# Performance work log

Measured on AMD Instinct MI355X. Metric: run time of the kernel, lower is better.

The kernel has to match this reference:

```python
import math
import jax, jax.numpy as jnp
import numpy as np

EMBED_DIM = 1024
ZDIM = 128
CHUNK = 2048
DSTATE = 16
DT_RANK = math.ceil(EMBED_DIM / 16)  # 64


def silu(x):
    return x * jax.nn.sigmoid(x)


def rmsnorm(x, w, eps=1e-5):
    var = jnp.mean(x * x, axis=-1, keepdims=True)
    return x * jax.lax.rsqrt(var + eps) * w


def _rotary(v, sin, cos):
    # v: (n, d) -> rotate half
    x1, x2 = jnp.split(v, 2, axis=-1)
    return jnp.concatenate([x1 * cos - x2 * sin, x2 * cos + x1 * sin], axis=-1)


def rel_pos_bias(alpha, beta, n):
    half = ZDIM // 2
    freqs = jnp.exp(jnp.arange(half, dtype=jnp.float32) * (-math.log(10000.0) / half))
    ang = jnp.arange(n, dtype=jnp.float32)[:, None] * freqs[None, :]
    sin, cos = jnp.sin(ang), jnp.cos(ang)
    a = _rotary(jnp.broadcast_to(alpha, (n, ZDIM)), sin, cos)
    b = _rotary(jnp.broadcast_to(beta, (n, ZDIM)), sin, cos)
    return jnp.einsum('mk,nk->mn', a, b)


def s6(u, xproj_w, dt_w, dt_b, A_log, D_p):
    # Mamba-style selective scan. u: (B, L, D)
    x_dbl = u @ xproj_w.T  # (B,L,dt_rank+2*N)
    dt, Bm, Cm = jnp.split(x_dbl, [DT_RANK, DT_RANK + DSTATE], axis=-1)
    dt = jax.nn.softplus(dt @ dt_w.T + dt_b)  # (B,L,D)
    A = -jnp.exp(A_log)  # (D,N)

    def step(h, inp):
        dt_t, B_t, C_t, u_t = inp  # (B,D),(B,N),(B,N),(B,D)
        dA = jnp.exp(dt_t[..., None] * A)  # (B,D,N)
        h = dA * h + (dt_t * u_t)[..., None] * B_t[:, None, :]
        y = jnp.einsum('bdn,bn->bd', h, C_t)
        return h, y

    B, L, D = u.shape
    h0 = jnp.zeros((B, D, DSTATE), u.dtype)
    xs = (dt.transpose(1, 0, 2), Bm.transpose(1, 0, 2), Cm.transpose(1, 0, 2), u.transpose(1, 0, 2))
    _, ys = jax.lax.scan(step, h0, xs)  # ys: (L,B,D)
    return ys.transpose(1, 0, 2) + u * D_p


def setup_inputs() -> dict:
    key = jax.random.key(0)
    ks = jax.random.split(key, 12)
    std = 0.02
    B, L, D = 2, 4096, EMBED_DIM
    f32 = jnp.float32
    inp = {
        'x': jax.random.normal(ks[0], (B, L, D), f32),
        'norm_w': jnp.ones((D,), f32),
        'v_w': jax.random.normal(ks[1], (D, D), f32) * std,
        'v_b': jnp.zeros((D,), f32),
        'mx_w': jax.random.normal(ks[2], (ZDIM + D + 2 * D, D), f32) * std,
        'mx_b': jnp.zeros((ZDIM + 3 * D,), f32),
        'h_w': jax.random.normal(ks[3], (D, D), f32) * std,
        'h_b': jnp.zeros((D,), f32),
        'gamma': jax.random.normal(ks[4], (2, ZDIM), f32) * std,
        'beta': jnp.zeros((2, ZDIM), f32),
        'alpha_rb': jax.random.normal(ks[5], (1, ZDIM), f32) * std,
        'beta_rb': jax.random.normal(ks[6], (1, ZDIM), f32) * std,
        'xproj_w': jax.random.normal(ks[7], (DT_RANK + 2 * DSTATE, D), f32) * std,
        'dt_w': jax.random.normal(ks[8], (D, DT_RANK), f32) * std,
        'dt_b': jnp.full((D,), -4.6, f32),  # softplus -> dt ~ 0.01
        'A_log': jnp.log(jnp.broadcast_to(jnp.arange(1, DSTATE + 1, dtype=f32), (D, DSTATE))),
        'D_p': jnp.ones((D,), f32),
    }
    return inp


def reference(x, norm_w, v_w, v_b, mx_w, mx_b, h_w, h_b, gamma, beta,
              alpha_rb, beta_rb, xproj_w, dt_w, dt_b, A_log, D_p):
    B, L, D = x.shape
    residual = x
    xn = rmsnorm(x, norm_w)
    v = silu(xn @ v_w.T + v_b)                       # (B,L,hdim)
    mx = silu(s6(xn, xproj_w, dt_w, dt_b, A_log, D_p))
    base = mx @ mx_w.T + mx_b                        # (B,L,zdim+hdim+2D)
    u, zr, hx = jnp.split(base, [D, D + ZDIM + D], axis=-1)
    u = jax.nn.sigmoid(u)
    zr = silu(zr)
    z, r = jnp.split(zr, [ZDIM], axis=-1)
    z = z[..., None, :] * gamma + beta               # (B,L,2,Z)
    q, k = z[..., 0, :], z[..., 1, :]
    c = min(CHUNK, L)
    nc = L // c
    qh = q.reshape(B, nc, c, ZDIM) * (ZDIM ** -0.5)
    kh = k.reshape(B, nc, c, ZDIM)
    vh = v.reshape(B, nc, c, D)
    bias = rel_pos_bias(alpha_rb, beta_rb, c)        # (c,c)
    mask = jnp.triu(jnp.full((c, c), -jnp.inf, jnp.float32), 1)
    qk = jnp.einsum('bnqz,bnkz->bnqk', qh, kh) + bias + mask
    attn = jax.nn.softmax(qk.astype(jnp.float32), axis=-1).astype(qk.dtype)
    h = jnp.einsum('bnqk,bnkd->bnqd', attn, vh).reshape(B, L, D)
    h = silu(hx + (h * r) @ h_w.T + h_b)
    return residual + u * (h - residual)
```

## Files before the change

kernel.cpp:

```cpp
#include <hip/hip_runtime.h>
#include <hip/hip_bf16.h>
#include <math.h>

#define EMBED 1024
#define LSEQ 4096
#define BATCH 2
#define ZD 128
#define CHUNKC 2048
#define NSTATE 16
#define DTR 64
#define XDBL_W 96
#define NSEG 64
#define TSEG 64

typedef __attribute__((ext_vector_type(8))) short bf16x8;
typedef __attribute__((ext_vector_type(4))) float f32x4;

__device__ __forceinline__ float sigmoidf_(float x){ return 1.f/(1.f+__expf(-x)); }
__device__ __forceinline__ float siluf_(float x){ return x/(1.f+__expf(-x)); }
__device__ __forceinline__ __hip_bfloat16 tobf(float x){ return __float2bfloat16(x); }
__device__ __forceinline__ float frombf(__hip_bfloat16 x){ return __bfloat162float(x); }

__device__ __forceinline__ void gload_lds16(const void* g, void* l) {
  __builtin_amdgcn_global_load_lds(
      (const __attribute__((address_space(1))) unsigned int*)g,
      (__attribute__((address_space(3))) unsigned int*)l, 16, 0, 0);
}

__global__ __launch_bounds__(256) void prep_k(
    const float* __restrict__ v_w, const float* __restrict__ xproj_w,
    const float* __restrict__ h_w, const float* __restrict__ dt_w,
    const float* __restrict__ mx_w,
    const float* __restrict__ alpha, const float* __restrict__ beta,
    __hip_bfloat16* __restrict__ wcat, __hip_bfloat16* __restrict__ hwb,
    __hip_bfloat16* __restrict__ dtwb, __hip_bfloat16* __restrict__ mxwb,
    float* __restrict__ gtab)
{
  int b = blockIdx.x, tid = threadIdx.x;
  if (b < 5440) {
    const float* s; __hip_bfloat16* d; int idx;
    if (b < 1024)      { idx = (b*256+tid)*4;        s = v_w + idx;      d = wcat + idx; }
    else if (b < 1120) { idx = ((b-1024)*256+tid)*4; s = xproj_w + idx;  d = wcat + (1<<20) + idx; }
    else if (b < 1152) { idx = ((b-1120)*256+tid)*4; s = nullptr;        d = wcat + (1<<20) + 96*1024 + idx; }
    else if (b < 2176) { idx = ((b-1152)*256+tid)*4; s = h_w + idx;      d = hwb + idx; }
    else if (b < 2240) { idx = ((b-2176)*256+tid)*4; s = dt_w + idx;     d = dtwb + idx; }
    else               { idx = ((b-2240)*256+tid)*4; s = mx_w + idx;     d = mxwb + idx; }
    if (s) {
      float4 v = *(const float4*)s;
      d[0]=tobf(v.x); d[1]=tobf(v.y); d[2]=tobf(v.z); d[3]=tobf(v.w);
    } else {
      d[0]=tobf(0.f); d[1]=tobf(0.f); d[2]=tobf(0.f); d[3]=tobf(0.f);
    }
    return;
  }
  __shared__ float P[64], Q[64], F[64];
  if (tid < 64) {
    float a1=alpha[tid], a2=alpha[64+tid], b1=beta[tid], b2=beta[64+tid];
    P[tid]=a1*b1+a2*b2;
    Q[tid]=a2*b1-a1*b2;
    F[tid]=expf(-0.14391156831f*(float)tid);
  }
  __syncthreads();
  int d = (b-5440)*256 + tid;
  if (d < CHUNKC) {
    float s=0.f;
    for (int j=0;j<64;++j){
      float th = (float)d * F[j];
      float sn, cs;
      sincosf(th, &sn, &cs);
      s += P[j]*cs - Q[j]*sn;
    }
    gtab[d]=s;
  }
}

__global__ __launch_bounds__(256) void rmsnorm_k(const float* __restrict__ x,
                                                 const float* __restrict__ w,
                                                 __hip_bfloat16* __restrict__ xnb) {
  size_t row = blockIdx.x;
  const float* px = x + row*EMBED;
  int tid = threadIdx.x;
  float4 xv = *(const float4*)(px + tid*4);
  float ss = xv.x*xv.x + xv.y*xv.y + xv.z*xv.z + xv.w*xv.w;
  #pragma unroll
  for (int off=32; off; off>>=1) ss += __shfl_down(ss, off, 64);
  __shared__ float red[4];
  if ((tid&63)==0) red[tid>>6]=ss;
  __syncthreads();
  float tot = red[0]+red[1]+red[2]+red[3];
  float scale = rsqrtf(tot*(1.f/EMBED) + 1e-5f);
  float4 wv = *(const float4*)(w + tid*4);
  __hip_bfloat16* pb = xnb + row*EMBED + tid*4;
  pb[0]=tobf(xv.x*scale*wv.x); pb[1]=tobf(xv.y*scale*wv.y);
  pb[2]=tobf(xv.z*scale*wv.z); pb[3]=tobf(xv.w*scale*wv.w);
}

template<bool FINAL>
__global__ __launch_bounds__(256) void seg_scan_k(
    const float* __restrict__ xbc,
    const __hip_bfloat16* __restrict__ dtv,
    const __hip_bfloat16* __restrict__ xnu,
    const float* __restrict__ A_log,
    const float* __restrict__ D_p,
    const float* __restrict__ segInit,
    float* __restrict__ segP,
    float* __restrict__ segH,
    __hip_bfloat16* __restrict__ mx)
{
  int bx = blockIdx.x;
  int seg = bx >> 3;
  int grp = bx & 7;
  int b = grp >> 2;
  int d = (grp & 3)*256 + threadIdx.x;
  int ch = b*EMBED + d;
  int tid = threadIdx.x;
  int tbase = seg*TSEG;

  float A[NSTATE], h[NSTATE], P[NSTATE];
  #pragma unroll
  for (int n=0;n<NSTATE;++n){
    A[n] = -__expf(A_log[(size_t)d*NSTATE+n]);
    P[n] = 1.f;
  }
  if (FINAL) {
    const float* si = segInit + ((size_t)seg*2048 + ch)*NSTATE;
    #pragma unroll
    for (int n=0;n<NSTATE;++n) h[n] = si[n];
  } else {
    #pragma unroll
    for (int n=0;n<NSTATE;++n) h[n] = 0.f;
  }
  float Dp = FINAL ? D_p[d] : 0.f;

  __shared__ float BCb[8][32];
  const float* xd = xbc + ((size_t)b*LSEQ + tbase)*32;
  const __hip_bfloat16* pdt = dtv + ((size_t)b*LSEQ + tbase)*EMBED + d;
  const __hip_bfloat16* pu  = xnu + ((size_t)b*LSEQ + tbase)*EMBED + d;
  __hip_bfloat16* pmx = mx + ((size_t)b*LSEQ + tbase)*EMBED + d;

  for (int t0=0; t0<TSEG; t0+=8) {
    __syncthreads();
    { int tt = tid>>5, jj = tid&31;
      BCb[tt][jj] = xd[(size_t)(t0+tt)*32 + jj]; }
    __syncthreads();
    #pragma unroll
    for (int tt=0; tt<8; ++tt) {
      int t = t0 + tt;
      float dtt = frombf(pdt[(size_t)t*EMBED]);
      float ut  = frombf(pu[(size_t)t*EMBED]);
      float du = dtt*ut;
      float y = 0.f;
      #pragma unroll
      for (int n=0;n<NSTATE;++n){
        float dA = __expf(dtt*A[n]);
        h[n] = dA*h[n] + du*BCb[tt][n];
        if (!FINAL) P[n] *= dA;
        if (FINAL)  y += h[n]*BCb[tt][16+n];
      }
      if (FINAL) pmx[(size_t)t*EMBED] = tobf(siluf_(y + ut*Dp));
    }
  }
  if (!FINAL) {
    float* pp = segP + ((size_t)seg*2048 + ch)*NSTATE;
    float* ph = segH + ((size_t)seg*2048 + ch)*NSTATE;
    #pragma unroll
    for (int n=0;n<NSTATE;n+=4){
      *(float4*)(pp+n) = make_float4(P[n],P[n+1],P[n+2],P[n+3]);
      *(float4*)(ph+n) = make_float4(h[n],h[n+1],h[n+2],h[n+3]);
    }
  }
}

__global__ __launch_bounds__(256) void seg_combine_k(const float* __restrict__ segP,
                                                     const float* __restrict__ segH,
                                                     float* __restrict__ segInit) {
  int idx = blockIdx.x*256 + threadIdx.x;
  float H = 0.f;
  for (int s=0; s<NSEG; ++s) {
    size_t o = (size_t)s*32768 + idx;
    float Pv = segP[o], hl = segH[o];
    segInit[o] = H;
    H = Pv*H + hl;
  }
}

__global__ __launch_bounds__(256) void softmax_k(const __hip_bfloat16* __restrict__ S,
                                                 __hip_bfloat16* __restrict__ Sb) {
  size_t row = blockIdx.x;
  const __hip_bfloat16* p = S + row*CHUNKC;
  __hip_bfloat16* po = Sb + row*CHUNKC;
  int tid = threadIdx.x;
  int r = (int)(row & (CHUNKC-1));
  int nb = (r >> 8) + 1;
  int kcl = ((r >> 7) + 1) << 7;
  float v[8];
  float m = -1e30f;
  #pragma unroll
  for (int i=0;i<8;++i){
    if (i < nb) {
      float t = frombf(p[tid + i*256]);
      v[i] = (i*256 + tid <= r) ? t : -1e30f;
    } else v[i] = -1e30f;
    m = fmaxf(m, v[i]);
  }
  #pragma unroll
  for (int off=32; off; off>>=1) m = fmaxf(m, __shfl_down(m, off, 64));
  __shared__ float red[4];
  if ((tid&63)==0) red[tid>>6]=m;
  __syncthreads();
  m = fmaxf(fmaxf(red[0],red[1]),fmaxf(red[2],red[3]));
  float s=0.f;
  #pragma unroll
  for (int i=0;i<8;++i){ v[i]=__expf(v[i]-m); s+=v[i]; }
  #pragma unroll
  for (int off=32; off; off>>=1) s += __shfl_down(s, off, 64);
  __syncthreads();
  if ((tid&63)==0) red[tid>>6]=s;
  __syncthreads();
  s = red[0]+red[1]+red[2]+red[3];
  float inv = 1.f/s;
  #pragma unroll
  for (int i=0;i<8;++i){
    int c = tid + i*256;
    if (c < kcl) po[c] = tobf(v[i]*inv);
  }
}

__global__ __launch_bounds__(256) void transpose_k(const unsigned short* __restrict__ vb,
                                                   unsigned short* __restrict__ VT) {
  __shared__ unsigned short t[64][68];
  int tid = threadIdx.x;
  int tr = tid>>4;
  int tc = (tid&15)*4;
  int c0 = blockIdx.x*64, r0 = blockIdx.y*64;
  #pragma unroll
  for (int it=0; it<4; ++it) {
    int r = it*16 + tr;
    ushort4 v = *(const ushort4*)(vb + (size_t)(r0+r)*EMBED + c0 + tc);
    t[r][tc+0]=v.x; t[r][tc+1]=v.y; t[r][tc+2]=v.z; t[r][tc+3]=v.w;
  }
  __syncthreads();
  int ch = r0 >> 11;
  int kb = r0 & 2047;
  #pragma unroll
  for (int it=0; it<4; ++it) {
    int nl = it*16 + tr;
    ushort4 o;
    o.x = t[tc+0][nl]; o.y = t[tc+1][nl]; o.z = t[tc+2][nl]; o.w = t[tc+3][nl];
    *(ushort4*)(VT + ((size_t)ch*EMBED + c0 + nl)*CHUNKC + kb + tc) = o;
  }
}

struct MEp {
  const float* bias; const float* gtab; const float* gamma; const float* beta2;
  __hip_bfloat16* ug; __hip_bfloat16* qo; __hip_bfloat16* ko; __hip_bfloat16* ro; __hip_bfloat16* hxo;
  const __hip_bfloat16* rb; const __hip_bfloat16* hxb; const __hip_bfloat16* ub;
  const float* resid; float* outp;
  __hip_bfloat16* Cb; int ldc;
  float* f32o; __hip_bfloat16* bf16o;
};

__device__ __forceinline__ void xcd_swz(int& bx, int& by) {
  const int gx = gridDim.x;
  const int nwg = gx*gridDim.y;
  const int lin = by*gx + bx;
  const int qq = nwg >> 3, rr = nwg & 7;
  const int xcd = lin & 7, pos = lin >> 3;
  const int base = (xcd < rr) ? xcd*(qq+1) : rr*(qq+1) + (xcd-rr)*qq;
  const int lg = base + pos;
  bx = lg % gx; by = lg / gx;
}

#define MBM 128
#define MBK 64

template<int EPI, bool TRIK, bool SWZ>
__global__ __launch_bounds__(256, 3) void mgemm_k(
    const __hip_bfloat16* __restrict__ A, int lda, long long sAz,
    const __hip_bfloat16* __restrict__ B, int ldb, long long sBz,
    int K, MEp ep)
{
  __shared__ __attribute__((aligned(16))) short As[2][MBM*MBK];
  __shared__ __attribute__((aligned(16))) short Bs[2][MBM*MBK];
  const int tid = threadIdx.x;
  const int wv = tid>>6, lane = tid&63;
  const int z = blockIdx.z;
  A += (size_t)z * sAz;
  B += (size_t)z * sBz;
  int bx = blockIdx.x, by = blockIdx.y;
  if constexpr (SWZ) xcd_swz(bx, by);
  const int m0 = by*MBM, n0 = bx*MBM;
  if constexpr (EPI==2) { if (n0 > m0 + (MBM-1)) return; }
  const int r8 = lane>>3, g8 = lane&7;
  const int csrc = g8 ^ r8;
  const int wr = wv>>1, wc = wv&1;
  const int fr = lane&15, qv = lane>>4;
  const int x7 = fr & 7;

  int Ktot = K;
  if constexpr (TRIK) { int km = m0 + MBM; Ktot = km < K ? km : K; }
  const int nt = Ktot / MBK;

  f32x4 acc[4][4] = {};

  const __hip_bfloat16* Ag = A + (size_t)(m0 + wv*32 + r8)*lda + csrc*8;
  const __hip_bfloat16* Bg = B + (size_t)(n0 + wv*32 + r8)*ldb + csrc*8;

  auto stage = [&](int buf, int t){
    const int k0 = t*MBK;
    short* Al = &As[buf][wv*32*MBK];
    short* Bl = &Bs[buf][wv*32*MBK];
    #pragma unroll
    for (int j=0;j<4;++j)
      gload_lds16(Ag + (size_t)(j*8)*lda + k0, Al + j*8*MBK);
    #pragma unroll
    for (int j=0;j<4;++j)
      gload_lds16(Bg + (size_t)(j*8)*ldb + k0, Bl + j*8*MBK);
  };

  stage(0, 0);
  if (nt > 1) {
    stage(1, 1);
    asm volatile("s_waitcnt vmcnt(8)" ::: "memory");
  } else {
    asm volatile("s_waitcnt vmcnt(0)" ::: "memory");
  }
  __builtin_amdgcn_sched_barrier(0);
  __builtin_amdgcn_s_barrier();

  for (int t=0; t<nt; ++t) {
    const int cur = t & 1;
    const short* Ab = &As[cur][0];
    const short* Bb = &Bs[cur][0];
    #pragma unroll
    for (int kk=0; kk<2; ++kk) {
      const int pos8 = ((kk*4 + qv) ^ x7) * 8;
      bf16x8 af[4], bfr[4];
      #pragma unroll
      for (int mi=0;mi<4;++mi)
        af[mi] = *(const bf16x8*)&Ab[(wr*64 + mi*16 + fr)*MBK + pos8];
      #pragma unroll
      for (int ni=0;ni<4;++ni)
        bfr[ni] = *(const bf16x8*)&Bb[(wc*64 + ni*16 + fr)*MBK + pos8];
      #pragma unroll
      for (int mi=0;mi<4;++mi)
        #pragma unroll
        for (int ni=0;ni<4;++ni)
          acc[mi][ni] = __builtin_amdgcn_mfma_f32_16x16x32_bf16(af[mi], bfr[ni], acc[mi][ni], 0,0,0);
    }
    if (t+1 >= nt) break;
    __builtin_amdgcn_sched_barrier(0);
    __builtin_amdgcn_s_barrier();
    if (t+2 < nt) {
      stage(cur, t+2);
      asm volatile("s_waitcnt vmcnt(8)" ::: "memory");
    } else {
      asm volatile("s_waitcnt vmcnt(0)" ::: "memory");
    }
    __builtin_amdgcn_sched_barrier(0);
    __builtin_amdgcn_s_barrier();
  }

  const int vr = (lane>>4)*4;
  #pragma unroll
  for (int mi=0;mi<4;++mi) {
    #pragma unroll
    for (int v=0; v<4; ++v) {
      const int row = m0 + wr*64 + mi*16 + vr + v;
      #pragma unroll
      for (int ni=0;ni<4;++ni) {
        const int col = n0 + wc*64 + ni*16 + fr;
        float val = acc[mi][ni][v];
        if constexpr (EPI==1) {
          val += ep.bias[col];
          if (col < 1024) {
            ep.ug[(size_t)row*EMBED + col] = tobf(sigmoidf_(val));
          } else if (col < 1152) {
            int jj = col - 1024;
            float zz = siluf_(val);
            ep.qo[(size_t)row*ZD + jj] = tobf((zz*ep.gamma[jj] + ep.beta2[jj]) * 0.08838834764831845f);
            ep.ko[(size_t)row*ZD + jj] = tobf(zz*ep.gamma[128+jj] + ep.beta2[128+jj]);
          } else if (col < 2176) {
            ep.ro[(size_t)row*EMBED + (col-1152)] = tobf(siluf_(val));
          } else {
            ep.hxo[(size_t)row*EMBED + (col-2176)] = tobf(val);
          }
        } else if constexpr (EPI==2) {
          __hip_bfloat16* Sp = ep.Cb + (size_t)z*CHUNKC*CHUNKC;
          if (col <= row) Sp[(size_t)row*CHUNKC + col] = tobf(val + ep.gtab[row-col]);
        } else if constexpr (EPI==3) {
          size_t gr = (size_t)z*CHUNKC + row;
          ep.Cb[gr*EMBED + col] = tobf(val * frombf(ep.rb[gr*EMBED + col]));
        } else if constexpr (EPI==4) {
          float zz = val + ep.bias[col] + frombf(ep.hxb[(size_t)row*EMBED + col]);
          float hh = siluf_(zz);
          float res = ep.resid[(size_t)row*EMBED + col];
          ep.outp[(size_t)row*EMBED + col] = res + frombf(ep.ub[(size_t)row*EMBED + col])*(hh-res);
        } else if constexpr (EPI==6) {
          float zv = val + ep.bias[col];
          ep.bf16o[(size_t)row*EMBED + col] = tobf((zv > 15.f) ? zv : log1pf(__expf(zv)));
        } else {
          if (col < 1024) {
            ep.Cb[(size_t)row*ep.ldc + col] = tobf(siluf_(val + ep.bias[col]));
          } else {
            int jj = col - 1024;
            if (jj < DTR)          ep.bf16o[(size_t)row*DTR + jj] = tobf(val);
            else if (jj < XDBL_W)  ep.f32o[(size_t)row*32 + (jj - DTR)] = val;
          }
        }
      }
    }
  }
}

extern "C" void kernel_launch(void* const* d_in, const int* in_sizes, int n_in,
                              void* d_out, int out_size, void* d_ws, size_t ws_size,
                              hipStream_t stream) {
  const float* x       = (const float*)d_in[0];
  const float* norm_w  = (const float*)d_in[1];
  const float* v_w     = (const float*)d_in[2];
  const float* v_b     = (const float*)d_in[3];
  const float* mx_w    = (const float*)d_in[4];
  const float* mx_b    = (const float*)d_in[5];
  const float* h_w     = (const float*)d_in[6];
  const float* h_b     = (const float*)d_in[7];
  const float* gamma   = (const float*)d_in[8];
  const float* beta    = (const float*)d_in[9];
  const float* alpha_rb= (const float*)d_in[10];
  const float* beta_rb = (const float*)d_in[11];
  const float* xproj_w = (const float*)d_in[12];
  const float* dt_w    = (const float*)d_in[13];
  const float* dt_b    = (const float*)d_in[14];
  const float* A_log   = (const float*)d_in[15];
  const float* D_p     = (const float*)d_in[16];
  float* out = (float*)d_out;

  float* ws = (float*)d_ws;
  size_t off = 0;
  auto alloc = [&](size_t n){ float* p = ws + off; off += n; return p; };
  const size_t BL2 = (size_t)BATCH*LSEQ;

  float* sbzone  = alloc(BL2*EMBED);
  float* scratch = alloc((size_t)2*CHUNKC*CHUNKC*2);
  float* xbc     = alloc(BL2*32);
  float* gtab    = alloc(CHUNKC);
  auto balloc = [&](size_t nbf){ __hip_bfloat16* p = (__hip_bfloat16*)(ws + off); off += (nbf+1)/2; return p; };
  __hip_bfloat16* xnb   = balloc(BL2*EMBED);
  __hip_bfloat16* vbufb = balloc(BL2*EMBED);
  __hip_bfloat16* mxb   = balloc(BL2*EMBED);
  __hip_bfloat16* qb    = balloc(BL2*ZD);
  __hip_bfloat16* kb    = balloc(BL2*ZD);
  __hip_bfloat16* ugb   = balloc(BL2*EMBED);
  __hip_bfloat16* rbb   = balloc(BL2*EMBED);
  __hip_bfloat16* hxbb  = balloc(BL2*EMBED);
  __hip_bfloat16* hrb   = balloc(BL2*EMBED);
  __hip_bfloat16* xdblb = balloc(BL2*DTR);
  __hip_bfloat16* wcat  = balloc((size_t)1152*EMBED);
  __hip_bfloat16* mxwb  = balloc((size_t)3200*EMBED);
  __hip_bfloat16* hwb   = balloc((size_t)EMBED*EMBED);
  __hip_bfloat16* dtwb  = balloc((size_t)EMBED*DTR);

  __hip_bfloat16* dtbb = (__hip_bfloat16*)scratch;
  float* segP    = scratch + BL2*EMBED;
  float* segH    = segP + (size_t)NSEG*2048*NSTATE;
  float* segInit = segH + (size_t)NSEG*2048*NSTATE;
  __hip_bfloat16* S  = (__hip_bfloat16*)scratch;
  __hip_bfloat16* Sb = (__hip_bfloat16*)sbzone;
  __hip_bfloat16* VT = xnb;

  prep_k<<<5448, 256, 0, stream>>>(v_w, xproj_w, h_w, dt_w, mx_w,
                                   alpha_rb, beta_rb,
                                   wcat, hwb, dtwb, mxwb, gtab);

  rmsnorm_k<<<(int)BL2, 256, 0, stream>>>(x, norm_w, xnb);

  MEp ep;

  ep = {}; ep.bias = v_b; ep.Cb = vbufb; ep.ldc = EMBED;
  ep.f32o = xbc; ep.bf16o = xdblb;
  mgemm_k<7,false,true><<<dim3(1152/MBM, BL2/MBM), 256, 0, stream>>>(
      xnb, EMBED, 0, wcat, EMBED, 0, EMBED, ep);

  ep = {}; ep.bias = dt_b; ep.bf16o = dtbb;
  mgemm_k<6,false,true><<<dim3(EMBED/MBM, BL2/MBM), 256, 0, stream>>>(
      xdblb, DTR, 0, dtwb, DTR, 0, DTR, ep);

  seg_scan_k<false><<<NSEG*8, 256, 0, stream>>>(xbc, dtbb, xnb, A_log, D_p,
                                                nullptr, segP, segH, nullptr);
  seg_combine_k<<<128, 256, 0, stream>>>(segP, segH, segInit);
  seg_scan_k<true><<<NSEG*8, 256, 0, stream>>>(xbc, dtbb, xnb, A_log, D_p,
                                               segInit, nullptr, nullptr, mxb);

  transpose_k<<<dim3(EMBED/64, BL2/64), 256, 0, stream>>>(
      (const unsigned short*)vbufb, (unsigned short*)VT);

  ep = {}; ep.bias = mx_b; ep.gamma = gamma; ep.beta2 = beta;
  ep.ug = ugb; ep.qo = qb; ep.ko = kb; ep.ro = rbb; ep.hxo = hxbb;
  mgemm_k<1,false,true><<<dim3(3200/MBM, BL2/MBM), 256, 0, stream>>>(
      mxb, EMBED, 0, mxwb, EMBED, 0, EMBED, ep);

  ep = {}; ep.gtab = gtab; ep.Cb = S;
  mgemm_k<2,false,true><<<dim3(CHUNKC/MBM, CHUNKC/MBM, 4), 256, 0, stream>>>(
      qb, ZD, (long long)CHUNKC*ZD, kb, ZD, (long long)CHUNKC*ZD, ZD, ep);

  softmax_k<<<4*CHUNKC, 256, 0, stream>>>(S, Sb);

  ep = {}; ep.rb = rbb; ep.Cb = hrb;
  mgemm_k<3,true,true><<<dim3(EMBED/MBM, CHUNKC/MBM, 4), 256, 0, stream>>>(
      Sb, CHUNKC, (long long)CHUNKC*CHUNKC, VT, CHUNKC, (long long)EMBED*CHUNKC, CHUNKC, ep);

  ep = {}; ep.bias = h_b; ep.hxb = hxbb; ep.ub = ugb; ep.resid = x; ep.outp = out;
  mgemm_k<4,false,true><<<dim3(EMBED/MBM, BL2/MBM), 256, 0, stream>>>(
      hrb, EMBED, 0, hwb, EMBED, 0, EMBED, ep);
}
```

Before: 492.9 us.

## Replace double-buffered GEMM staging with single buffer to raise occupancy

The GEMM kernel drops its double-buffered LDS staging and explicit vmcnt-based prefetch pipeline. Each K-tile is now loaded into a single LDS buffer and followed by a barrier. This halves LDS use per block and raises the launch_bounds occupancy hint from 3 to 4 blocks. The bet is that more resident blocks will hide load latency better than the in-block prefetch did, at the cost of exposing global-load latency on every iteration within a block.

```diff
diff --git a/kernel.cpp b/kernel.cpp
--- a/kernel.cpp
+++ b/kernel.cpp
@@ -275,13 +275,13 @@
 #define MBK 64
 
 template<int EPI, bool TRIK, bool SWZ>
-__global__ __launch_bounds__(256, 3) void mgemm_k(
+__global__ __launch_bounds__(256, 4) void mgemm_k(
     const __hip_bfloat16* __restrict__ A, int lda, long long sAz,
     const __hip_bfloat16* __restrict__ B, int ldb, long long sBz,
     int K, MEp ep)
 {
-  __shared__ __attribute__((aligned(16))) short As[2][MBM*MBK];
-  __shared__ __attribute__((aligned(16))) short Bs[2][MBM*MBK];
+  __shared__ __attribute__((aligned(16))) short As[MBM*MBK];
+  __shared__ __attribute__((aligned(16))) short Bs[MBM*MBK];
   const int tid = threadIdx.x;
   const int wv = tid>>6, lane = tid&63;
   const int z = blockIdx.z;
@@ -306,10 +306,10 @@
   const __hip_bfloat16* Ag = A + (size_t)(m0 + wv*32 + r8)*lda + csrc*8;
   const __hip_bfloat16* Bg = B + (size_t)(n0 + wv*32 + r8)*ldb + csrc*8;
 
-  auto stage = [&](int buf, int t){
+  auto stage = [&](int t){
     const int k0 = t*MBK;
-    short* Al = &As[buf][wv*32*MBK];
-    short* Bl = &Bs[buf][wv*32*MBK];
+    short* Al = &As[wv*32*MBK];
+    short* Bl = &Bs[wv*32*MBK];
     #pragma unroll
     for (int j=0;j<4;++j)
       gload_lds16(Ag + (size_t)(j*8)*lda + k0, Al + j*8*MBK);
@@ -318,47 +318,26 @@
       gload_lds16(Bg + (size_t)(j*8)*ldb + k0, Bl + j*8*MBK);
   };
 
-  stage(0, 0);
-  if (nt > 1) {
-    stage(1, 1);
-    asm volatile("s_waitcnt vmcnt(8)" ::: "memory");
-  } else {
-    asm volatile("s_waitcnt vmcnt(0)" ::: "memory");
-  }
-  __builtin_amdgcn_sched_barrier(0);
-  __builtin_amdgcn_s_barrier();
-
   for (int t=0; t<nt; ++t) {
-    const int cur = t & 1;
-    const short* Ab = &As[cur][0];
-    const short* Bb = &Bs[cur][0];
+    stage(t);
+    __syncthreads();
     #pragma unroll
     for (int kk=0; kk<2; ++kk) {
       const int pos8 = ((kk*4 + qv) ^ x7) * 8;
       bf16x8 af[4], bfr[4];
       #pragma unroll
       for (int mi=0;mi<4;++mi)
-        af[mi] = *(const bf16x8*)&Ab[(wr*64 + mi*16 + fr)*MBK + pos8];
+        af[mi] = *(const bf16x8*)&As[(wr*64 + mi*16 + fr)*MBK + pos8];
       #pragma unroll
       for (int ni=0;ni<4;++ni)
-        bfr[ni] = *(const bf16x8*)&Bb[(wc*64 + ni*16 + fr)*MBK + pos8];
+        bfr[ni] = *(const bf16x8*)&Bs[(wc*64 + ni*16 + fr)*MBK + pos8];
       #pragma unroll
       for (int mi=0;mi<4;++mi)
         #pragma unroll
         for (int ni=0;ni<4;++ni)
           acc[mi][ni] = __builtin_amdgcn_mfma_f32_16x16x32_bf16(af[mi], bfr[ni], acc[mi][ni], 0,0,0);
     }
-    if (t+1 >= nt) break;
-    __builtin_amdgcn_sched_barrier(0);
-    __builtin_amdgcn_s_barrier();
-    if (t+2 < nt) {
-      stage(cur, t+2);
-      asm volatile("s_waitcnt vmcnt(8)" ::: "memory");
-    } else {
-      asm volatile("s_waitcnt vmcnt(0)" ::: "memory");
-    }
-    __builtin_amdgcn_sched_barrier(0);
-    __builtin_amdgcn_s_barrier();
+    if (t+1 < nt) __syncthreads();
   }
 
   const int vr = (lane>>4)*4;
```

Result: faster. 414.4 us (-15.9%).
